# Performance work log

Measured on AMD Instinct MI355X. Metric: run time of the kernel, lower is better.

Reference implementation:

```python
import jax, jax.numpy as jnp
import numpy as np
from jax import lax

EPS_DIST = 1e-6   # matches 1/(distances + 1e-6)
EPS_SQRT = 1e-12  # guard sqrt at zero


def setup_inputs() -> dict:
    key = jax.random.key(0)
    kq, ks = jax.random.split(key)
    query = jax.random.normal(kq, (2048, 32, 16), dtype=jnp.float32)
    support = jax.random.normal(ks, (65536, 32, 16), dtype=jnp.float32)
    return {"query": query, "support": support, "k": 16}


def reference(query, support, k):
    # Flatten (N, D, H) -> (N, D*H)
    q = query.reshape(query.shape[0], -1)   # (N_q, F)
    s = support.reshape(support.shape[0], -1)  # (N_s, F)
    # Euclidean distances via ||q||^2 + ||s||^2 - 2 q s^T
    q2 = jnp.sum(q * q, axis=1, keepdims=True)          # (N_q, 1)
    s2 = jnp.sum(s * s, axis=1)                          # (N_s,)
    d2 = q2 + s2[None, :] - 2.0 * (q @ s.T)              # (N_q, N_s)
    dist = jnp.sqrt(jnp.maximum(d2, EPS_SQRT))           # (N_q, N_s)
    # k smallest distances (sorted ascending, like sklearn kneighbors)
    neg_topk, indices = lax.top_k(-dist, k)              # (N_q, k)
    dist_k = -neg_topk
    sim = 1.0 / (dist_k + EPS_DIST)
    weights = sim / jnp.sum(sim, axis=1, keepdims=True)
    return indices, weights.astype(jnp.float32)
```

## Files before the change

kernel.cpp:

```cpp
#include <hip/hip_runtime.h>
#include <math.h>
#include <stdint.h>

#define NQ   2048
#define NS   65536
#define FDIM 512
#define KSEL 16
#define LDA  132
#define LDB  320
#define LDT  132

typedef _Float16 f16x8 __attribute__((ext_vector_type(8)));
typedef float    f32x16 __attribute__((ext_vector_type(16)));

#define GLL16(dst, src)                                                        \
  __builtin_amdgcn_global_load_lds(                                            \
      (const __attribute__((address_space(1))) void*)(src),                    \
      (__attribute__((address_space(3))) void*)(dst), 16, 0, 0)

#define BAR_NOVM() asm volatile("s_waitcnt lgkmcnt(0)\ns_barrier" ::: "memory")

__global__ void knn_norms(const float* __restrict__ q, const float* __restrict__ s,
                          float* __restrict__ q2, float* __restrict__ s2) {
  int wid  = (int)blockIdx.x * 4 + ((int)threadIdx.x >> 6);
  int lane = threadIdx.x & 63;
  if (wid >= NQ + NS) return;
  const float* src = (wid < NQ) ? (q + (size_t)wid * FDIM)
                                : (s + (size_t)(wid - NQ) * FDIM);
  float acc = 0.f;
#pragma unroll
  for (int j = 0; j < FDIM / 256; ++j) {
    float4 v = *(const float4*)&src[(lane + 64 * j) * 4];
    acc = fmaf(v.x, v.x, acc); acc = fmaf(v.y, v.y, acc);
    acc = fmaf(v.z, v.z, acc); acc = fmaf(v.w, v.w, acc);
  }
#pragma unroll
  for (int off = 32; off; off >>= 1) acc += __shfl_xor(acc, off, 64);
  if (lane == 0) {
    if (wid < NQ) q2[wid] = acc;
    else          s2[wid - NQ] = acc;
  }
}

__global__ void knn_prep(const float* __restrict__ q, const float* __restrict__ s,
                         float* __restrict__ q2, float* __restrict__ s2,
                         _Float16* __restrict__ qh, _Float16* __restrict__ ql,
                         _Float16* __restrict__ sh, _Float16* __restrict__ slo) {
  const int wgl = (int)blockIdx.x * 4 + ((int)threadIdx.x >> 6);
  const int ln  = threadIdx.x & 63;
  const int lm  = ln & 31;
  const int lh  = ln >> 5;
  constexpr int NRBQ = NQ / 32;
  constexpr int NRB  = (NQ + NS) / 32;
  if (wgl >= NRB) return;
  const bool isq = wgl < NRBQ;
  const int rb = isq ? wgl : wgl - NRBQ;
  const float* src = (isq ? q : s) + ((size_t)rb * 32 + lm) * FDIM + lh * 8;
  _Float16* hp = (isq ? qh : sh)  + (size_t)rb * (32 * FDIM);
  _Float16* lp = (isq ? ql : slo) + (size_t)rb * (32 * FDIM);
  const float scale = isq ? -2.f : 1.f;
  float acc = 0.f;
#pragma unroll 4
  for (int kb = 0; kb < FDIM / 16; ++kb) {
    float4 v0 = *(const float4*)&src[kb * 16];
    float4 v1 = *(const float4*)&src[kb * 16 + 4];
    const float x[8] = {v0.x, v0.y, v0.z, v0.w, v1.x, v1.y, v1.z, v1.w};
    f16x8 hv, lv;
#pragma unroll
    for (int j = 0; j < 8; ++j) {
      acc = fmaf(x[j], x[j], acc);
      float xs = x[j] * scale;
      _Float16 h = (_Float16)xs;
      hv[j] = h;
      lv[j] = (_Float16)(xs - (float)h);
    }
    *(f16x8*)&hp[(size_t)kb * 512 + ln * 8] = hv;
    *(f16x8*)&lp[(size_t)kb * 512 + ln * 8] = lv;
  }
  acc += __shfl_xor(acc, 32, 64);
  if (ln < 32) {
    if (isq) q2[rb * 32 + lm] = acc;
    else     s2[rb * 32 + lm] = acc;
  }
}

template <int CT>
__device__ __forceinline__ void sel_slice2(
    const f32x16 (&acc)[4][2], float (&ld)[KSEL], int (&li)[KSEL],
    float (*scr)[257], const float* s2c,
    int wv, int lm, int lh, int srow, int shalf, int s0, int slp) {
  BAR_NOVM();
  if ((wv & 3) == slp) {
    const int c = lm;
    const float s2v = s2c[slp * 64 + CT * 32 + c];
    const int rb = (wv >> 2) * 128;
#pragma unroll
    for (int rt = 0; rt < 4; ++rt)
#pragma unroll
      for (int r = 0; r < 16; ++r) {
        const int row = rb + rt * 32 + (r & 3) + 8 * (r >> 2) + 4 * lh;
        scr[c][row] = acc[rt][CT][r] + s2v;
      }
  }
  BAR_NOVM();
  const int cbase = s0 + slp * 64 + CT * 32 + shalf * 16;
  for (int c = 0; c < 16; ++c) {
    const float ev = scr[shalf * 16 + c][srow];
    if (ev < ld[KSEL - 1]) {
      bool lt[KSEL];
#pragma unroll
      for (int s = 0; s < KSEL; ++s) lt[s] = ev < ld[s];
      const int iv = cbase + c;
#pragma unroll
      for (int s = KSEL - 1; s >= 1; --s) {
        ld[s] = lt[s - 1] ? ld[s - 1] : (lt[s] ? ev : ld[s]);
        li[s] = lt[s - 1] ? li[s - 1] : (lt[s] ? iv : li[s]);
      }
      if (lt[0]) { ld[0] = ev; li[0] = iv; }
    }
  }
}

template <int NCHUNK>
__global__ __launch_bounds__(512, 2) void knn_phase1_mfma256(
    const _Float16* __restrict__ qh, const _Float16* __restrict__ ql,
    const _Float16* __restrict__ sh, const _Float16* __restrict__ sl_,
    const float* __restrict__ s2g,
    float* __restrict__ cand_e, int* __restrict__ cand_i) {
  constexpr int CHUNKSZ = NS / NCHUNK;
  constexpr int NST     = CHUNKSZ / 256;
  constexpr int NT      = NST * 32;
  constexpr int BUFH    = 16384;

  __shared__ __align__(16) _Float16 stg[3 * BUFH];
  __shared__ __align__(16) float scr[32][257];
  __shared__ __align__(16) float s2all[CHUNKSZ];

  const int tid = threadIdx.x;
  const int wv  = tid >> 6;
  const int ln  = tid & 63;
  const int lm  = ln & 31;
  const int lh  = ln >> 5;
  const int wr  = wv >> 2;
  const int wc  = wv & 3;
  const int q0  = (int)blockIdx.x * 256;
  const int chunk = blockIdx.y;
  const int rbA  = q0 >> 5;
  const int rbB0 = chunk * (CHUNKSZ >> 5);

  float ld[KSEL]; int li[KSEL];
#pragma unroll
  for (int s = 0; s < KSEL; ++s) { ld[s] = INFINITY; li[s] = 0x7fffffff; }
  const int srow  = tid >> 1;
  const int shalf = tid & 1;
  const size_t lo = (size_t)ln * 8;

  {
    float4 v = *(const float4*)&s2g[(size_t)chunk * CHUNKSZ + tid * 4];
    *(float4*)&s2all[tid * 4] = v;
    asm volatile("s_waitcnt lgkmcnt(0)" ::: "memory");
  }

  auto STAGE = [&](int b, int t) {
    const int st_ = t >> 5, kb_ = t & 31;
    _Float16* d = stg + b * BUFH;
    const size_t ak = ((size_t)(rbA + wv) * 32 + kb_) * 512 + lo;
    const size_t bk = ((size_t)(rbB0 + st_ * 8 + wv) * 32 + kb_) * 512 + lo;
    GLL16(d +         wv * 512, qh  + ak);
    GLL16(d +  4096 + wv * 512, ql  + ak);
    GLL16(d +  8192 + wv * 512, sh  + bk);
    GLL16(d + 12288 + wv * 512, sl_ + bk);
  };

  STAGE(0, 0);
  STAGE(1, 1);
  int b0 = 0, b1 = 1, b2 = 2;

#pragma unroll 1
  for (int st = 0; st < NST; ++st) {
    const int s0 = chunk * CHUNKSZ + st * 256;

    f32x16 acc[4][2];
#pragma unroll
    for (int rt = 0; rt < 4; ++rt)
#pragma unroll
      for (int ct = 0; ct < 2; ++ct)
#pragma unroll
        for (int r = 0; r < 16; ++r) acc[rt][ct][r] = 0.f;

#pragma unroll 1
    for (int kb = 0; kb < 32; ++kb) {
      const int t = st * 32 + kb;
      if (t < NT - 1) { asm volatile("s_waitcnt vmcnt(4)" ::: "memory"); }
      else            { asm volatile("s_waitcnt vmcnt(0)" ::: "memory"); }
      __builtin_amdgcn_s_barrier();
      __builtin_amdgcn_sched_barrier(0);
      if (t + 2 < NT) STAGE(b2, t + 2);

      const _Float16* base = stg + b0 * BUFH;
      f16x8 bh0 = *(const f16x8*)&base[ 8192 + (wc * 2 + 0) * 512 + ln * 8];
      f16x8 bh1 = *(const f16x8*)&base[ 8192 + (wc * 2 + 1) * 512 + ln * 8];
      f16x8 bl0 = *(const f16x8*)&base[12288 + (wc * 2 + 0) * 512 + ln * 8];
      f16x8 bl1 = *(const f16x8*)&base[12288 + (wc * 2 + 1) * 512 + ln * 8];
#pragma unroll
      for (int rt = 0; rt < 4; ++rt) {
        f16x8 ahf = *(const f16x8*)&base[       (wr * 4 + rt) * 512 + ln * 8];
        f16x8 alf = *(const f16x8*)&base[4096 + (wr * 4 + rt) * 512 + ln * 8];
        acc[rt][0] = __builtin_amdgcn_mfma_f32_32x32x16_f16(ahf, bh0, acc[rt][0], 0, 0, 0);
        acc[rt][1] = __builtin_amdgcn_mfma_f32_32x32x16_f16(ahf, bh1, acc[rt][1], 0, 0, 0);
        acc[rt][0] = __builtin_amdgcn_mfma_f32_32x32x16_f16(ahf, bl0, acc[rt][0], 0, 0, 0);
        acc[rt][1] = __builtin_amdgcn_mfma_f32_32x32x16_f16(ahf, bl1, acc[rt][1], 0, 0, 0);
        acc[rt][0] = __builtin_amdgcn_mfma_f32_32x32x16_f16(alf, bh0, acc[rt][0], 0, 0, 0);
        acc[rt][1] = __builtin_amdgcn_mfma_f32_32x32x16_f16(alf, bh1, acc[rt][1], 0, 0, 0);
      }
      const int tmp = b0; b0 = b1; b1 = b2; b2 = tmp;
    }

#pragma unroll 1
    for (int slp = 0; slp < 4; ++slp) {
      sel_slice2<0>(acc, ld, li, scr, s2all + st * 256, wv, lm, lh, srow, shalf, s0, slp);
      sel_slice2<1>(acc, ld, li, scr, s2all + st * 256, wv, lm, lh, srow, shalf, s0, slp);
    }
  }

  const size_t base =
      ((size_t)(q0 + srow) * NCHUNK + chunk) * (2 * KSEL) + shalf * KSEL;
#pragma unroll
  for (int j = 0; j < KSEL; ++j) {
    cand_e[base + j] = ld[j];
    cand_i[base + j] = li[j];
  }
}

template <int NCHUNK, int HALVES>
__global__ __launch_bounds__(256, 2) void knn_phase1(
    const float* __restrict__ query, const float* __restrict__ support,
    const float* __restrict__ s2g,
    float* __restrict__ cand_e, int* __restrict__ cand_i) {
  constexpr int CHUNKSZ = NS / NCHUNK;
  constexpr int NST = CHUNKSZ / 256;

  __shared__ __align__(16) float AsT[16][LDA];
  __shared__ __align__(16) float BsT[16 * LDB];
  __shared__ __align__(16) float scrT[64][LDT];
  __shared__ float s2s[256];

  const int tid = threadIdx.x;
  const int tx  = tid & 15;
  const int ty  = tid >> 4;
  const int q0  = (int)blockIdx.x * 128;
  const int chunk = blockIdx.y;

  float ld[KSEL]; int li[KSEL];
#pragma unroll
  for (int s = 0; s < KSEL; ++s) { ld[s] = INFINITY; li[s] = 0x7fffffff; }
  const int  srow  = (HALVES == 2) ? (tid >> 1) : tid;
  const int  shalf = (HALVES == 2) ? (tid & 1) : 0;
  const bool scan_active = (HALVES == 2) || (tid < 128);

  for (int st = 0; st < NST; ++st) {
    const int s0 = chunk * CHUNKSZ + st * 256;
    s2s[tid] = s2g[s0 + tid];

    float acc[8][16];
#pragma unroll
    for (int i = 0; i < 8; ++i)
#pragma unroll
      for (int j = 0; j < 16; ++j) acc[i][j] = 0.f;

    float4 pa[2], pb[4];
    const int rr = tid >> 2, cq = tid & 3, cc = cq << 2;

#pragma unroll
    for (int p = 0; p < 2; ++p)
      pa[p] = *(const float4*)&query[(size_t)(q0 + rr + 64 * p) * FDIM + cc];
#pragma unroll
    for (int p = 0; p < 4; ++p)
      pb[p] = *(const float4*)&support[(size_t)(s0 + rr + 64 * p) * FDIM + cc];

    for (int kb = 0; kb < FDIM / 16; ++kb) {
      __syncthreads();
#pragma unroll
      for (int p = 0; p < 2; ++p) {
        const int r = rr + 64 * p;
        const float v[4] = {pa[p].x, pa[p].y, pa[p].z, pa[p].w};
#pragma unroll
        for (int j = 0; j < 4; ++j) AsT[cq * 4 + j][r] = v[j];
      }
#pragma unroll
      for (int p = 0; p < 4; ++p) {
        const int r  = rr + 64 * p;
        const int pc = 20 * (r >> 4) + (r & 15);
        const float v[4] = {pb[p].x, pb[p].y, pb[p].z, pb[p].w};
#pragma unroll
        for (int j = 0; j < 4; ++j) BsT[(cq * 4 + j) * LDB + pc] = v[j];
      }
      if (kb + 1 < FDIM / 16) {
        const int kc = (kb + 1) * 16 + cc;
#pragma unroll
        for (int p = 0; p < 2; ++p)
          pa[p] = *(const float4*)&query[(size_t)(q0 + rr + 64 * p) * FDIM + kc];
#pragma unroll
        for (int p = 0; p < 4; ++p)
          pb[p] = *(const float4*)&support[(size_t)(s0 + rr + 64 * p) * FDIM + kc];
      }
      __syncthreads();
#pragma unroll 4
      for (int kk = 0; kk < 16; ++kk) {
        float4 a0 = *(const float4*)&AsT[kk][ty * 8];
        float4 a1 = *(const float4*)&AsT[kk][ty * 8 + 4];
        const float* brow = &BsT[kk * LDB + 20 * tx];
        float4 b0 = *(const float4*)&brow[0];
        float4 b1 = *(const float4*)&brow[4];
        float4 b2 = *(const float4*)&brow[8];
        float4 b3 = *(const float4*)&brow[12];
        const float a[8]  = {a0.x, a0.y, a0.z, a0.w, a1.x, a1.y, a1.z, a1.w};
        const float b[16] = {b0.x, b0.y, b0.z, b0.w, b1.x, b1.y, b1.z, b1.w,
                             b2.x, b2.y, b2.z, b2.w, b3.x, b3.y, b3.z, b3.w};
#pragma unroll
        for (int i = 0; i < 8; ++i)
#pragma unroll
          for (int j = 0; j < 16; ++j)
            acc[i][j] = fmaf(a[i], b[j], acc[i][j]);
      }
    }

#pragma unroll 1
    for (int sl = 0; sl < 4; ++sl) {
      __syncthreads();
      if ((tx >> 2) == sl) {
        const int csb = (tx & 3) * 16;
#pragma unroll
        for (int j = 0; j < 16; ++j) {
          const float s2v = s2s[tx * 16 + j];
          float4 v0, v1;
          v0.x = fmaf(-2.f, acc[0][j], s2v);
          v0.y = fmaf(-2.f, acc[1][j], s2v);
          v0.z = fmaf(-2.f, acc[2][j], s2v);
          v0.w = fmaf(-2.f, acc[3][j], s2v);
          v1.x = fmaf(-2.f, acc[4][j], s2v);
          v1.y = fmaf(-2.f, acc[5][j], s2v);
          v1.z = fmaf(-2.f, acc[6][j], s2v);
          v1.w = fmaf(-2.f, acc[7][j], s2v);
          *(float4*)&scrT[csb + j][ty * 8]     = v0;
          *(float4*)&scrT[csb + j][ty * 8 + 4] = v1;
        }
      }
      __syncthreads();
      if (scan_active) {
        const int cbase = s0 + sl * 64 + shalf * 32;
        const int ccount = (HALVES == 2) ? 32 : 64;
        const int coff   = (HALVES == 2) ? shalf * 32 : 0;
        for (int c = 0; c < ccount; ++c) {
          const float ev = scrT[coff + c][srow];
          if (ev < ld[KSEL - 1]) {
            bool lt[KSEL];
#pragma unroll
            for (int s = 0; s < KSEL; ++s) lt[s] = ev < ld[s];
            const int iv = cbase + c;
#pragma unroll
            for (int s = KSEL - 1; s >= 1; --s) {
              ld[s] = lt[s - 1] ? ld[s - 1] : (lt[s] ? ev : ld[s]);
              li[s] = lt[s - 1] ? li[s - 1] : (lt[s] ? iv : li[s]);
            }
            if (lt[0]) { ld[0] = ev; li[0] = iv; }
          }
        }
      }
    }
  }

  if (scan_active) {
    const size_t base =
        ((size_t)(q0 + srow) * NCHUNK + chunk) * (HALVES * KSEL) + shalf * KSEL;
#pragma unroll
    for (int j = 0; j < KSEL; ++j) {
      cand_e[base + j] = ld[j];
      cand_i[base + j] = li[j];
    }
  }
}

template <int NCAND>
__global__ __launch_bounds__(64) void knn_phase2(
    const float* __restrict__ cand_e, const int* __restrict__ cand_i,
    const float* __restrict__ q2g, float* __restrict__ out) {
  constexpr int SLOTS = NCAND / 64;
  __shared__ float wd[KSEL];
  __shared__ int   wi[KSEL];

  const int q    = blockIdx.x;
  const int lane = threadIdx.x;
  const float q2 = q2g[q];
  const float* ce = cand_e + (size_t)q * NCAND;
  const int*   ci = cand_i + (size_t)q * NCAND;

  float d[SLOTS]; int idx[SLOTS];
#pragma unroll
  for (int s = 0; s < SLOTS; ++s) {
    d[s]   = q2 + ce[lane + 64 * s];
    idx[s] = ci[lane + 64 * s];
  }

  for (int r = 0; r < KSEL; ++r) {
    float bd = INFINITY; int bi = 0x7fffffff;
#pragma unroll
    for (int s = 0; s < SLOTS; ++s) {
      bool better = (d[s] < bd) || (d[s] == bd && idx[s] < bi);
      if (better) { bd = d[s]; bi = idx[s]; }
    }
#pragma unroll
    for (int off = 32; off; off >>= 1) {
      float od = __shfl_xor(bd, off, 64);
      int   oi = __shfl_xor(bi, off, 64);
      if (od < bd || (od == bd && oi < bi)) { bd = od; bi = oi; }
    }
#pragma unroll
    for (int s = 0; s < SLOTS; ++s)
      if (idx[s] == bi) { d[s] = INFINITY; idx[s] = 0x7fffffff; }
    if (lane == 0) { wd[r] = bd; wi[r] = bi; }
  }
  __syncthreads();

  float sim = 0.f;
  if (lane < KSEL) {
    const float dist = sqrtf(fmaxf(wd[lane], 1e-12f));
    sim = 1.f / (dist + 1e-6f);
  }
  float tot = sim;
#pragma unroll
  for (int off = 8; off; off >>= 1) tot += __shfl_xor(tot, off, 64);
  if (lane < KSEL) {
    out[(size_t)q * KSEL + lane] = (float)wi[lane];
    out[(size_t)NQ * KSEL + (size_t)q * KSEL + lane] = sim / tot;
  }
}

extern "C" void kernel_launch(void* const* d_in, const int* in_sizes, int n_in,
                              void* d_out, int out_size, void* d_ws, size_t ws_size,
                              hipStream_t stream) {
  const float* query   = (const float*)d_in[0];
  const float* support = (const float*)d_in[1];
  float* out = (float*)d_out;

  float* q2     = (float*)d_ws;
  float* s2     = q2 + NQ;
  float* cand_e = s2 + NS;

  constexpr int NCHUNK = 32;
  const size_t cand_elems = (size_t)NQ * NCHUNK * 2 * KSEL;
  const size_t plane_off  = (size_t)(NQ + NS) + 2 * cand_elems;
  const size_t half_elems = 2 * (size_t)(NQ + NS) * FDIM;
  const size_t need_mfma  = plane_off * 4 + half_elems * 2;
  const size_t need2 = (size_t)(NQ + NS + 2 * NQ * NCHUNK * 2 * KSEL) * 4;

  if (ws_size >= need_mfma) {
    int* cand_i = (int*)(cand_e + cand_elems);
    _Float16* qh  = (_Float16*)((float*)d_ws + plane_off);
    _Float16* ql  = qh + (size_t)NQ * FDIM;
    _Float16* shp = ql + (size_t)NQ * FDIM;
    _Float16* slp = shp + (size_t)NS * FDIM;
    knn_prep<<<(NQ + NS) / (32 * 4), 256, 0, stream>>>(query, support, q2, s2,
                                                       qh, ql, shp, slp);
    dim3 g1(NQ / 256, NCHUNK);
    knn_phase1_mfma256<NCHUNK><<<g1, 512, 0, stream>>>(qh, ql, shp, slp, s2,
                                                       cand_e, cand_i);
    knn_phase2<NCHUNK * 2 * KSEL><<<NQ, 64, 0, stream>>>(cand_e, cand_i, q2, out);
  } else {
    knn_norms<<<(NQ + NS) / 4, 256, 0, stream>>>(query, support, q2, s2);
    if (ws_size >= need2) {
      int* cand_i = (int*)(cand_e + (size_t)NQ * NCHUNK * 2 * KSEL);
      dim3 g1(NQ / 128, NCHUNK);
      knn_phase1<NCHUNK, 2><<<g1, 256, 0, stream>>>(query, support, s2, cand_e, cand_i);
      knn_phase2<NCHUNK * 2 * KSEL><<<NQ, 64, 0, stream>>>(cand_e, cand_i, q2, out);
    } else {
      int* cand_i = (int*)(cand_e + (size_t)NQ * NCHUNK * KSEL);
      dim3 g1(NQ / 128, NCHUNK);
      knn_phase1<NCHUNK, 1><<<g1, 256, 0, stream>>>(query, support, s2, cand_e, cand_i);
      knn_phase2<NCHUNK * KSEL><<<NQ, 64, 0, stream>>>(cand_e, cand_i, q2, out);
    }
  }
}
```

Baseline: 905.8 us.

## Split K-step into two phases with interleaved LDS loads, barriers and setprio

Restructures the inner MFMA loop into two halves. Each half loads its A fragments from LDS, then issues an MFMA burst under raised wave priority, with extra barriers and the next global-to-LDS stage issued mid-iteration. The vmcnt wait moves to the middle of the step so global loads overlap more of the compute. This is a ping-pong style schedule that trades more barriers per iteration for better overlap of LDS reads, global loads and matrix ops across waves. The barrier placement around buffer reuse with the triple buffer must stay correct.

Measured after the change: 867.6 us. 1.04x faster.

```diff
diff --git a/kernel.cpp b/kernel.cpp
--- a/kernel.cpp
+++ b/kernel.cpp
@@ -19,6 +19,8 @@
       (__attribute__((address_space(3))) void*)(dst), 16, 0, 0)
 
 #define BAR_NOVM() asm volatile("s_waitcnt lgkmcnt(0)\ns_barrier" ::: "memory")
+
+#define MFMA16(a, b, c) __builtin_amdgcn_mfma_f32_32x32x16_f16((a), (b), (c), 0, 0, 0)
 
 __global__ void knn_norms(const float* __restrict__ q, const float* __restrict__ s,
                           float* __restrict__ q2, float* __restrict__ s2) {
@@ -174,6 +176,8 @@
 
   STAGE(0, 0);
   STAGE(1, 1);
+  asm volatile("s_waitcnt vmcnt(4)" ::: "memory");
+  __builtin_amdgcn_s_barrier();
   int b0 = 0, b1 = 1, b2 = 2;
 
 #pragma unroll 1
@@ -191,28 +195,61 @@
 #pragma unroll 1
     for (int kb = 0; kb < 32; ++kb) {
       const int t = st * 32 + kb;
-      if (t < NT - 1) { asm volatile("s_waitcnt vmcnt(4)" ::: "memory"); }
-      else            { asm volatile("s_waitcnt vmcnt(0)" ::: "memory"); }
-      __builtin_amdgcn_s_barrier();
-      __builtin_amdgcn_sched_barrier(0);
-      if (t + 2 < NT) STAGE(b2, t + 2);
-
       const _Float16* base = stg + b0 * BUFH;
+
       f16x8 bh0 = *(const f16x8*)&base[ 8192 + (wc * 2 + 0) * 512 + ln * 8];
       f16x8 bh1 = *(const f16x8*)&base[ 8192 + (wc * 2 + 1) * 512 + ln * 8];
       f16x8 bl0 = *(const f16x8*)&base[12288 + (wc * 2 + 0) * 512 + ln * 8];
       f16x8 bl1 = *(const f16x8*)&base[12288 + (wc * 2 + 1) * 512 + ln * 8];
-#pragma unroll
-      for (int rt = 0; rt < 4; ++rt) {
-        f16x8 ahf = *(const f16x8*)&base[       (wr * 4 + rt) * 512 + ln * 8];
-        f16x8 alf = *(const f16x8*)&base[4096 + (wr * 4 + rt) * 512 + ln * 8];
-        acc[rt][0] = __builtin_amdgcn_mfma_f32_32x32x16_f16(ahf, bh0, acc[rt][0], 0, 0, 0);
-        acc[rt][1] = __builtin_amdgcn_mfma_f32_32x32x16_f16(ahf, bh1, acc[rt][1], 0, 0, 0);
-        acc[rt][0] = __builtin_amdgcn_mfma_f32_32x32x16_f16(ahf, bl0, acc[rt][0], 0, 0, 0);
-        acc[rt][1] = __builtin_amdgcn_mfma_f32_32x32x16_f16(ahf, bl1, acc[rt][1], 0, 0, 0);
-        acc[rt][0] = __builtin_amdgcn_mfma_f32_32x32x16_f16(alf, bh0, acc[rt][0], 0, 0, 0);
-        acc[rt][1] = __builtin_amdgcn_mfma_f32_32x32x16_f16(alf, bh1, acc[rt][1], 0, 0, 0);
-      }
+      f16x8 a0h = *(const f16x8*)&base[       (wr * 4 + 0) * 512 + ln * 8];
+      f16x8 a0l = *(const f16x8*)&base[4096 + (wr * 4 + 0) * 512 + ln * 8];
+      f16x8 a1h = *(const f16x8*)&base[       (wr * 4 + 1) * 512 + ln * 8];
+      f16x8 a1l = *(const f16x8*)&base[4096 + (wr * 4 + 1) * 512 + ln * 8];
+      if (t + 2 < NT) STAGE(b2, t + 2);
+      __builtin_amdgcn_s_barrier();
+      asm volatile("s_waitcnt lgkmcnt(0)" ::: "memory");
+      __builtin_amdgcn_sched_barrier(0);
+      __builtin_amdgcn_s_setprio(1);
+      acc[0][0] = MFMA16(a0h, bh0, acc[0][0]);
+      acc[0][1] = MFMA16(a0h, bh1, acc[0][1]);
+      acc[0][0] = MFMA16(a0h, bl0, acc[0][0]);
+      acc[0][1] = MFMA16(a0h, bl1, acc[0][1]);
+      acc[0][0] = MFMA16(a0l, bh0, acc[0][0]);
+      acc[0][1] = MFMA16(a0l, bh1, acc[0][1]);
+      acc[1][0] = MFMA16(a1h, bh0, acc[1][0]);
+      acc[1][1] = MFMA16(a1h, bh1, acc[1][1]);
+      acc[1][0] = MFMA16(a1h, bl0, acc[1][0]);
+      acc[1][1] = MFMA16(a1h, bl1, acc[1][1]);
+      acc[1][0] = MFMA16(a1l, bh0, acc[1][0]);
+      acc[1][1] = MFMA16(a1l, bh1, acc[1][1]);
+      __builtin_amdgcn_s_setprio(0);
+      __builtin_amdgcn_s_barrier();
+
+      f16x8 a2h = *(const f16x8*)&base[       (wr * 4 + 2) * 512 + ln * 8];
+      f16x8 a2l = *(const f16x8*)&base[4096 + (wr * 4 + 2) * 512 + ln * 8];
+      f16x8 a3h = *(const f16x8*)&base[       (wr * 4 + 3) * 512 + ln * 8];
+      f16x8 a3l = *(const f16x8*)&base[4096 + (wr * 4 + 3) * 512 + ln * 8];
+      if (t < NT - 2)      { asm volatile("s_waitcnt vmcnt(4)" ::: "memory"); }
+      else if (t == NT - 2){ asm volatile("s_waitcnt vmcnt(0)" ::: "memory"); }
+      __builtin_amdgcn_s_barrier();
+      asm volatile("s_waitcnt lgkmcnt(0)" ::: "memory");
+      __builtin_amdgcn_sched_barrier(0);
+      __builtin_amdgcn_s_setprio(1);
+      acc[2][0] = MFMA16(a2h, bh0, acc[2][0]);
+      acc[2][1] = MFMA16(a2h, bh1, acc[2][1]);
+      acc[2][0] = MFMA16(a2h, bl0, acc[2][0]);
+      acc[2][1] = MFMA16(a2h, bl1, acc[2][1]);
+      acc[2][0] = MFMA16(a2l, bh0, acc[2][0]);
+      acc[2][1] = MFMA16(a2l, bh1, acc[2][1]);
+      acc[3][0] = MFMA16(a3h, bh0, acc[3][0]);
+      acc[3][1] = MFMA16(a3h, bh1, acc[3][1]);
+      acc[3][0] = MFMA16(a3h, bl0, acc[3][0]);
+      acc[3][1] = MFMA16(a3h, bl1, acc[3][1]);
+      acc[3][0] = MFMA16(a3l, bh0, acc[3][0]);
+      acc[3][1] = MFMA16(a3l, bh1, acc[3][1]);
+      __builtin_amdgcn_s_setprio(0);
+      __builtin_amdgcn_s_barrier();
+
       const int tmp = b0; b0 = b1; b1 = b2; b2 = tmp;
     }
 
```
